# Performance work log

Hardware: AMD Instinct MI355X
Metric: run time of the kernel (lower is better)

## Reference

```python
import math
import jax, jax.numpy as jnp
import numpy as np

B, L, D = 2, 2048, 1024
NH = 16
HS = D // NH
BLOCK_SIZE = 2048


def setup_inputs() -> dict:
    key = jax.random.key(0)
    ks = jax.random.split(key, 4)
    x = jax.random.normal(ks[0], (B, L, D), dtype=jnp.float32)
    Wqkv = jax.random.normal(ks[1], (D, 3 * D), dtype=jnp.float32) * 0.02
    bqkv = jnp.zeros((3 * D,), dtype=jnp.float32)
    Wproj = jax.random.normal(ks[2], (D, D), dtype=jnp.float32) * 0.02
    bproj = jnp.zeros((D,), dtype=jnp.float32)
    Er = jax.random.normal(ks[3], (BLOCK_SIZE, HS), dtype=jnp.float32)
    return {"x": x, "Wqkv": Wqkv, "bqkv": bqkv, "Wproj": Wproj, "bproj": bproj, "Er": Er}


def _skew(QEr):
    # QEr: [B, nh, L, L]  (Music Transformer skew trick)
    b, nh, nr, nc = QEr.shape
    padded = jnp.pad(QEr, ((0, 0), (0, 0), (0, 0), (1, 0)))  # [B, nh, nr, nc+1]
    reshaped = padded.reshape(b, nh, nc + 1, nr)
    return reshaped[:, :, 1:, :]  # [B, nh, nr, nc]


def reference(x, Wqkv, bqkv, Wproj, bproj, Er):
    b, l, d = x.shape
    qkv = x @ Wqkv + bqkv  # [B, L, 3D]
    q, k, v = jnp.split(qkv, 3, axis=2)
    q = q.reshape(b, l, NH, HS).transpose(0, 2, 1, 3)  # [B, nh, L, hs]
    k = k.reshape(b, l, NH, HS).transpose(0, 2, 1, 3)
    v = v.reshape(b, l, NH, HS).transpose(0, 2, 1, 3)

    start = BLOCK_SIZE - l
    Er_t = Er[start:, :].T  # [hs, L]
    QEr = jnp.einsum('bhld,dm->bhlm', q, Er_t)  # [B, nh, L, L]
    Srel = _skew(QEr)

    QK_t = jnp.einsum('bhld,bhmd->bhlm', q, k)
    scale = 1.0 / math.sqrt(HS)
    att = (QK_t + Srel) * scale
    causal = jnp.tril(jnp.ones((l, l), dtype=bool))
    att = jnp.where(causal[None, None, :, :], att, jnp.float32(-jnp.inf))
    att = jax.nn.softmax(att, axis=-1)
    y = jnp.einsum('bhlm,bhmd->bhld', att, v)
    y = y.transpose(0, 2, 1, 3).reshape(b, l, d)
    return y @ Wproj + bproj
```

## Files before the change

kernel.cpp:

```cpp
#include <hip/hip_runtime.h>
#include <stdint.h>

#define BB 2
#define LL 2048
#define DD 1024
#define NHH 16
#define HSS 64

typedef __bf16 bf16x8 __attribute__((ext_vector_type(8)));
typedef float f32x4 __attribute__((ext_vector_type(4)));

__device__ __forceinline__ bf16x8 load8(const float* p) {
  float4 f0 = *(const float4*)p;
  float4 f1 = *(const float4*)(p + 4);
  bf16x8 v;
  v[0] = (__bf16)f0.x; v[1] = (__bf16)f0.y; v[2] = (__bf16)f0.z; v[3] = (__bf16)f0.w;
  v[4] = (__bf16)f1.x; v[5] = (__bf16)f1.y; v[6] = (__bf16)f1.z; v[7] = (__bf16)f1.w;
  return v;
}
__device__ __forceinline__ bf16x8 load8(const __bf16* p) {
  return *(const bf16x8*)p;
}

__device__ __forceinline__ void async_ld16(__bf16* lds_uniform_base,
                                           const __bf16* gptr_per_lane) {
  __builtin_amdgcn_global_load_lds(
      (const __attribute__((address_space(1))) void*)gptr_per_lane,
      (__attribute__((address_space(3))) void*)lds_uniform_base, 16, 0, 0);
}

__global__ void prep_k(const float* __restrict__ Wqkv, const float* __restrict__ x,
                       const float* __restrict__ Er, __bf16* __restrict__ WqkvT,
                       __bf16* __restrict__ xb, __bf16* __restrict__ Erb) {
  int tx = threadIdx.x, ty = threadIdx.y;
  int tid = ty * 32 + tx;
  if (blockIdx.z == 1) {
    if (blockIdx.x >= 2048) return;
    size_t off = ((size_t)blockIdx.x * 256 + tid) * 8;
    *(bf16x8*)&xb[off] = load8(&x[off]);
    return;
  }
  if (blockIdx.z == 2) {
    if (blockIdx.x >= 64) return;
    size_t off = ((size_t)blockIdx.x * 256 + tid) * 8;
    *(bf16x8*)&Erb[off] = load8(&Er[off]);
    return;
  }
  __shared__ __bf16 tile[32][33];
  int c0 = (blockIdx.x % 96) * 32, r0 = (blockIdx.x / 96) * 32;
#pragma unroll
  for (int i = ty; i < 32; i += 8)
    tile[i][tx] = (__bf16)Wqkv[(size_t)(r0 + i) * 3072 + c0 + tx];
  __syncthreads();
#pragma unroll
  for (int i = ty; i < 32; i += 8)
    WqkvT[(size_t)(c0 + i) * 1024 + r0 + tx] = tile[tx][i];
}

__global__ void tconv_k(const float* __restrict__ src, __bf16* __restrict__ dst,
                        int R, int C) {
  __shared__ __bf16 tile[32][33];
  int c0 = blockIdx.x * 32, r0 = blockIdx.y * 32;
  int tx = threadIdx.x, ty = threadIdx.y;
#pragma unroll
  for (int i = ty; i < 32; i += 8)
    tile[i][tx] = (__bf16)src[(size_t)(r0 + i) * C + c0 + tx];
  __syncthreads();
#pragma unroll
  for (int i = ty; i < 32; i += 8)
    dst[(size_t)(c0 + i) * R + r0 + tx] = tile[tx][i];
}

__global__ __launch_bounds__(256) void gemm_qkv_k(
    const __bf16* __restrict__ A, const __bf16* __restrict__ Bt,
    const float* __restrict__ bias, __bf16* __restrict__ Qo,
    __bf16* __restrict__ Ko, __bf16* __restrict__ Vto) {
  const int K = 1024;
  __shared__ __align__(16) __bf16 As[128 * 32];
  __shared__ __align__(16) __bf16 Bs[128 * 32];
  __shared__ __align__(16) __bf16 Vl[64 * 136];
  int t = threadIdx.x;
  int wave = t >> 6, lane = t & 63, qd = lane >> 4, lr = lane & 15;
  int m0 = blockIdx.y * 128, n0 = blockIdx.x * 128;
  int wm = (wave >> 1) * 64, wn = (wave & 1) * 64;
  f32x4 acc[4][4] = {};
  int srow = lane >> 2, sch = (lane & 3) * 8;
  const __bf16* Ab[2];
  const __bf16* Bb[2];
#pragma unroll
  for (int c = 0; c < 2; c++) {
    Ab[c] = A + (size_t)(m0 + (wave * 2 + c) * 16 + srow) * K + sch;
    Bb[c] = Bt + (size_t)(n0 + (wave * 2 + c) * 16 + srow) * K + sch;
  }
  for (int k0 = 0; k0 < K; k0 += 32) {
    __syncthreads();
#pragma unroll
    for (int c = 0; c < 2; c++) {
      async_ld16(&As[(wave * 2 + c) * 512], Ab[c] + k0);
      async_ld16(&Bs[(wave * 2 + c) * 512], Bb[c] + k0);
    }
    __syncthreads();
    bf16x8 af[4], bfr[4];
#pragma unroll
    for (int mt = 0; mt < 4; mt++)
      af[mt] = *(const bf16x8*)&As[(wm + mt * 16 + lr) * 32 + qd * 8];
#pragma unroll
    for (int nt = 0; nt < 4; nt++)
      bfr[nt] = *(const bf16x8*)&Bs[(wn + nt * 16 + lr) * 32 + qd * 8];
#pragma unroll
    for (int mt = 0; mt < 4; mt++)
#pragma unroll
      for (int nt = 0; nt < 4; nt++)
        acc[mt][nt] = __builtin_amdgcn_mfma_f32_16x16x32_bf16(af[mt], bfr[nt],
                                                              acc[mt][nt], 0, 0, 0);
  }
  float bvv[4];
#pragma unroll
  for (int nt = 0; nt < 4; nt++) bvv[nt] = bias[n0 + wn + nt * 16 + lr];

  if (n0 < 2 * DD) {
#pragma unroll
    for (int mt = 0; mt < 4; mt++)
#pragma unroll
      for (int nt = 0; nt < 4; nt++)
#pragma unroll
        for (int r = 0; r < 4; r++) {
          int row = m0 + wm + mt * 16 + qd * 4 + r;
          int col = n0 + wn + nt * 16 + lr;
          __bf16 bb = (__bf16)(acc[mt][nt][r] + bvv[nt]);
          int b = row >> 11, l = row & 2047;
          int h = (col >> 6) & 15, d = col & 63;
          if (col < DD) {
            Qo[(((size_t)(b * NHH + h)) * LL + l) * HSS + d] = bb;
          } else {
            Ko[(((size_t)(b * NHH + h)) * LL + l) * HSS + d] = bb;
          }
        }
  } else {
    int vb0 = n0 - 2 * DD;
    int bq = m0 >> 11, l0 = m0 & 2047;
    int vr = t >> 2, vc = (t & 3) * 8;
#pragma unroll
    for (int c = 0; c < 2; c++) {
      if ((wave & 1) == c) {
#pragma unroll
        for (int mt = 0; mt < 4; mt++)
#pragma unroll
          for (int nt = 0; nt < 4; nt++)
#pragma unroll
            for (int r = 0; r < 4; r++) {
              int vrow = nt * 16 + lr;
              int ml = wm + mt * 16 + qd * 4 + r;
              Vl[vrow * 136 + ml] = (__bf16)(acc[mt][nt][r] + bvv[nt]);
            }
      }
      __syncthreads();
      int h = (vb0 + c * 64) >> 6;
      __bf16* dst = Vto + (((size_t)(bq * NHH + h)) * HSS + vr) * LL + l0 + vc;
      const __bf16* src = &Vl[vr * 136 + vc];
#pragma unroll
      for (int u = 0; u < 4; u++)
        *(bf16x8*)(dst + u * 32) = *(const bf16x8*)(src + u * 32);
      __syncthreads();
    }
  }
}

__global__ __launch_bounds__(256) void gemm_proj_k(
    const __bf16* __restrict__ A, const __bf16* __restrict__ Bt,
    const float* __restrict__ bias, float* __restrict__ out) {
  const int K = 1024, N = 1024;
  __shared__ __align__(16) __bf16 As[128 * 32];
  __shared__ __align__(16) __bf16 Bs[64 * 32];
  int t = threadIdx.x;
  int wave = t >> 6, lane = t & 63, qd = lane >> 4, lr = lane & 15;
  int m0 = blockIdx.y * 128, n0 = blockIdx.x * 64;
  int wm = (wave >> 1) * 64, wn = (wave & 1) * 32;
  f32x4 acc[4][2] = {};
  int srow = lane >> 2, sch = (lane & 3) * 8;
  const __bf16* Ab[2];
  const __bf16* Bb;
#pragma unroll
  for (int c = 0; c < 2; c++)
    Ab[c] = A + (size_t)(m0 + (wave * 2 + c) * 16 + srow) * K + sch;
  Bb = Bt + (size_t)(n0 + wave * 16 + srow) * K + sch;

  for (int k0 = 0; k0 < K; k0 += 32) {
    __syncthreads();
#pragma unroll
    for (int c = 0; c < 2; c++)
      async_ld16(&As[(wave * 2 + c) * 512], Ab[c] + k0);
    async_ld16(&Bs[wave * 512], Bb + k0);
    __syncthreads();
    bf16x8 af[4], bfr[2];
#pragma unroll
    for (int mt = 0; mt < 4; mt++)
      af[mt] = *(const bf16x8*)&As[(wm + mt * 16 + lr) * 32 + qd * 8];
#pragma unroll
    for (int nt = 0; nt < 2; nt++)
      bfr[nt] = *(const bf16x8*)&Bs[(wn + nt * 16 + lr) * 32 + qd * 8];
#pragma unroll
    for (int mt = 0; mt < 4; mt++)
#pragma unroll
      for (int nt = 0; nt < 2; nt++)
        acc[mt][nt] = __builtin_amdgcn_mfma_f32_16x16x32_bf16(af[mt], bfr[nt],
                                                              acc[mt][nt], 0, 0, 0);
  }
  float bvv[2];
#pragma unroll
  for (int nt = 0; nt < 2; nt++) bvv[nt] = bias[n0 + wn + nt * 16 + lr];
#pragma unroll
  for (int mt = 0; mt < 4; mt++)
#pragma unroll
    for (int nt = 0; nt < 2; nt++)
#pragma unroll
      for (int r = 0; r < 4; r++) {
        int row = m0 + wm + mt * 16 + qd * 4 + r;
        int col = n0 + wn + nt * 16 + lr;
        out[(size_t)row * N + col] = acc[mt][nt][r] + bvv[nt];
      }
}

__global__ __launch_bounds__(256, 3) void flash_k(
    const __bf16* __restrict__ Qg, const __bf16* __restrict__ Kg,
    const __bf16* __restrict__ Vtg, const __bf16* __restrict__ Erb,
    __bf16* __restrict__ Po0, __bf16* __restrict__ Po1,
    float* __restrict__ Lp0, float* __restrict__ Lp1) {
  __shared__ __align__(16) __bf16 Kbuf[2][64 * 64];
  __shared__ __align__(16) __bf16 Vbuf[2][64 * 64];
  __shared__ __align__(16) __bf16 Pball[4][16 * 64];

  int bh = blockIdx.x;
  int tile = 31 - (int)blockIdx.y;
  int i0 = tile * 64;
  int niter = tile + 1;
  int mid = (niter + 1) >> 1;
  int it0 = (blockIdx.z == 0) ? 0 : mid;
  int it1 = (blockIdx.z == 0) ? mid : niter;
  const __bf16* Qh = Qg + (size_t)bh * LL * HSS;
  const __bf16* Kh = Kg + (size_t)bh * LL * HSS;
  const __bf16* Vth = Vtg + (size_t)bh * HSS * LL;
  int b = bh >> 4, h = bh & 15;
  int t = threadIdx.x, wave = t >> 6, lane = t & 63, qd = lane >> 4, lr = lane & 15;
  __bf16* Pb = &Pball[wave][0];
  int cbase = 48 - wave * 16;

  const float SC = 0.18033688011112042f;

  int lrow = lane >> 3;
  int lcol = ((lane & 7) ^ lrow) * 8;
  const __bf16* KsrcB[2];
  const __bf16* VsrcB[2];
#pragma unroll
  for (int c = 0; c < 2; c++) {
    int q = wave * 2 + c;
    KsrcB[c] = Kh + (size_t)(q * 8 + lrow) * HSS + lcol;
    VsrcB[c] = Vth + (size_t)(q * 8 + lrow) * LL + lcol;
  }

  int swA = (qd ^ (lr & 7)) * 8;
  int swB = ((qd + 4) ^ (lr & 7)) * 8;

  int hi8 = lr >> 3;
  int ib0 = 15 - qd * 4 + lr;
  int pb0 = qd * 256 + (lr & 7);
  int px0 = (qd & 1) * 4;
  int rowb = i0 + wave * 16 + qd * 4;

  bf16x8 aq[2];
  {
    const __bf16* qrow = Qh + (size_t)(i0 + wave * 16 + lr) * HSS + qd * 8;
    aq[0] = *(const bf16x8*)qrow;
    aq[1] = *(const bf16x8*)(qrow + 32);
  }
  f32x4 oacc[4] = {};
  float lsum[4] = {};

  int cur = 0;
  if (it0 < it1) {
    int j0 = it0 * 64;
#pragma unroll
    for (int c = 0; c < 2; c++) {
      async_ld16(&Kbuf[0][(wave * 2 + c) * 512], KsrcB[c] + (size_t)j0 * HSS);
      async_ld16(&Vbuf[0][(wave * 2 + c) * 512], VsrcB[c] + j0);
    }
  }
  __syncthreads();

  for (int it = it0; it < it1; ++it) {
    int j0 = it * 64;

    if (it + 1 < it1) {
      int jn = (it + 1) * 64;
#pragma unroll
      for (int c = 0; c < 2; c++) {
        async_ld16(&Kbuf[cur ^ 1][(wave * 2 + c) * 512], KsrcB[c] + (size_t)jn * HSS);
        async_ld16(&Vbuf[cur ^ 1][(wave * 2 + c) * 512], VsrcB[c] + jn);
      }
    }

    int ebase = LL - 64 - i0 + j0 + cbase + lr;
    int e[5];
#pragma unroll
    for (int ct = 0; ct < 5; ct++) {
      int v = ebase + ct * 16;
      e[ct] = (v < LL) ? v : (LL - 1);
    }
    bf16x8 ef[5];
#pragma unroll
    for (int ct = 0; ct < 5; ct++)
      ef[ct] = *(const bf16x8*)&Erb[(size_t)e[ct] * HSS + qd * 8];

    const __bf16* Kb = &Kbuf[cur][0];
    const __bf16* Vb = &Vbuf[cur][0];

    f32x4 sacc[4] = {};
    __builtin_amdgcn_s_setprio(1);
#pragma unroll
    for (int ct = 0; ct < 4; ct++) {
      bf16x8 bk0 = *(const bf16x8*)&Kb[(ct * 16 + lr) * 64 + swA];
      bf16x8 bk1 = *(const bf16x8*)&Kb[(ct * 16 + lr) * 64 + swB];
      sacc[ct] = __builtin_amdgcn_mfma_f32_16x16x32_bf16(aq[0], bk0, sacc[ct], 0, 0, 0);
      sacc[ct] = __builtin_amdgcn_mfma_f32_16x16x32_bf16(aq[1], bk1, sacc[ct], 0, 0, 0);
    }
    __builtin_amdgcn_s_setprio(0);

    f32x4 racc[5] = {};
    __builtin_amdgcn_s_setprio(1);
#pragma unroll
    for (int ct = 0; ct < 5; ct++)
      racc[ct] = __builtin_amdgcn_mfma_f32_16x16x32_bf16(aq[0], ef[ct], racc[ct], 0, 0, 0);
    __builtin_amdgcn_s_setprio(0);

    __builtin_amdgcn_sched_barrier(0);

#pragma unroll
    for (int ct = 0; ct < 5; ct++)
      ef[ct] = *(const bf16x8*)&Erb[(size_t)e[ct] * HSS + 32 + qd * 8];

    __builtin_amdgcn_s_setprio(1);
#pragma unroll
    for (int ct = 0; ct < 5; ct++)
      racc[ct] = __builtin_amdgcn_mfma_f32_16x16x32_bf16(aq[1], ef[ct], racc[ct], 0, 0, 0);
    __builtin_amdgcn_s_setprio(0);

    int dib = rowb - j0;
#pragma unroll
    for (int r = 0; r < 4; r++) {
      int bse = ib0 - r;
      int hi = bse >> 4;
      int idx = (qd * 16 + (bse & 15)) << 2;
      float sh[5];
#pragma unroll
      for (int ct = 0; ct < 5; ct++)
        sh[ct] = __int_as_float(
            __builtin_amdgcn_ds_bpermute(idx, __float_as_int(racc[ct][r])));
      int di = dib + r;
#pragma unroll
      for (int ct2 = 0; ct2 < 4; ct2++) {
        float rel = hi ? sh[ct2 + 1] : sh[ct2];
        float p = __builtin_exp2f((sacc[ct2][r] + rel) * SC);
        p = (ct2 * 16 + lr <= di) ? p : 0.f;
        __bf16 pb = (__bf16)p;
        lsum[r] += (float)pb;
        Pb[pb0 + r * 64 + (((2 * ct2 + hi8) ^ (px0 + r)) << 3)] = pb;
      }
    }

    bf16x8 ap0 = *(const bf16x8*)&Pb[lr * 64 + swA];
    bf16x8 ap1 = *(const bf16x8*)&Pb[lr * 64 + swB];
    __builtin_amdgcn_s_setprio(1);
#pragma unroll
    for (int dt = 0; dt < 4; dt++) {
      bf16x8 bv0 = *(const bf16x8*)&Vb[(dt * 16 + lr) * 64 + swA];
      bf16x8 bv1 = *(const bf16x8*)&Vb[(dt * 16 + lr) * 64 + swB];
      oacc[dt] = __builtin_amdgcn_mfma_f32_16x16x32_bf16(ap0, bv0, oacc[dt], 0, 0, 0);
      oacc[dt] = __builtin_amdgcn_mfma_f32_16x16x32_bf16(ap1, bv1, oacc[dt], 0, 0, 0);
    }
    __builtin_amdgcn_s_setprio(0);

    __syncthreads();
    cur ^= 1;
  }

#pragma unroll
  for (int r = 0; r < 4; r++) {
#pragma unroll
    for (int m = 1; m < 16; m <<= 1)
      lsum[r] += __shfl_xor(lsum[r], m, 64);
  }

  __bf16* Po = (blockIdx.z == 0) ? Po0 : Po1;
  float* Lp = (blockIdx.z == 0) ? Lp0 : Lp1;
#pragma unroll
  for (int r = 0; r < 4; r++) {
    int l = i0 + wave * 16 + qd * 4 + r;
    if (lr == 0) Lp[(size_t)bh * LL + l] = lsum[r];
#pragma unroll
    for (int dt = 0; dt < 4; dt++) {
      int d = dt * 16 + lr;
      Po[((size_t)(b * LL) + l) * DD + h * HSS + d] = (__bf16)oacc[dt][r];
    }
  }
}

__global__ void combine_k(const __bf16* __restrict__ Po0,
                          const __bf16* __restrict__ Po1,
                          const float* __restrict__ Lp0,
                          const float* __restrict__ Lp1,
                          __bf16* __restrict__ Y) {
  size_t f = ((size_t)blockIdx.x * 256 + threadIdx.x) * 8;
  int dfull = (int)(f & 1023);
  int h = dfull >> 6;
  int l = (int)((f >> 10) & 2047);
  int b = (int)(f >> 21);
  size_t lidx = ((size_t)(b * NHH + h)) * LL + l;
  float linv = 1.f / (Lp0[lidx] + Lp1[lidx]);
  bf16x8 a = *(const bf16x8*)&Po0[f];
  bf16x8 c = *(const bf16x8*)&Po1[f];
  bf16x8 o;
#pragma unroll
  for (int q = 0; q < 8; q++)
    o[q] = (__bf16)(((float)a[q] + (float)c[q]) * linv);
  *(bf16x8*)&Y[f] = o;
}

extern "C" void kernel_launch(void* const* d_in, const int* in_sizes, int n_in,
                              void* d_out, int out_size, void* d_ws, size_t ws_size,
                              hipStream_t stream) {
  const float* x = (const float*)d_in[0];
  const float* Wqkv = (const float*)d_in[1];
  const float* bqkv = (const float*)d_in[2];
  const float* Wproj = (const float*)d_in[3];
  const float* bproj = (const float*)d_in[4];
  const float* Er = (const float*)d_in[5];
  float* out = (float*)d_out;

  if (ws_size < 4u * 8388608u) return;

  uint8_t* w = (uint8_t*)d_ws;
  __bf16* Q = (__bf16*)w;  w += (size_t)BB * NHH * LL * HSS * 2;
  __bf16* Kt = (__bf16*)w; w += (size_t)BB * NHH * LL * HSS * 2;
  __bf16* Vt = (__bf16*)w; w += (size_t)BB * NHH * LL * HSS * 2;
  __bf16* Y = (__bf16*)w;  w += (size_t)BB * LL * DD * 2;

  __bf16* WqkvT = (__bf16*)d_out;
  __bf16* xb = (__bf16*)((uint8_t*)d_out + (size_t)3072 * 1024 * 2);
  __bf16* Erb = (__bf16*)((uint8_t*)d_out + (size_t)3072 * 1024 * 2 + (size_t)4096 * 1024 * 2);
  __bf16* Po1 = (__bf16*)d_out;
  float* Lp0 = (float*)((uint8_t*)d_out + (size_t)BB * LL * DD * 2);
  float* Lp1 = (float*)((uint8_t*)d_out + (size_t)BB * LL * DD * 2 + (size_t)BB * NHH * LL * 4);
  __bf16* Po0 = Y;
  __bf16* WprojT = Q;

  prep_k<<<dim3(3072, 1, 3), dim3(32, 8), 0, stream>>>(Wqkv, x, Er, WqkvT, xb, Erb);
  gemm_qkv_k<<<dim3(3072 / 128, 4096 / 128), 256, 0, stream>>>(
      xb, WqkvT, bqkv, Q, Kt, Vt);
  flash_k<<<dim3(BB * NHH, 32, 2), 256, 0, stream>>>(
      Q, Kt, Vt, Erb, Po0, Po1, Lp0, Lp1);
  combine_k<<<dim3(2048), 256, 0, stream>>>(Po0, Po1, Lp0, Lp1, Y);
  tconv_k<<<dim3(1024 / 32, 1024 / 32), dim3(32, 8), 0, stream>>>(Wproj, WprojT, 1024, 1024);
  gemm_proj_k<<<dim3(1024 / 64, 4096 / 128), 256, 0, stream>>>(Y, WprojT, bproj, out);
}
```

Before: 243.6 us.

## Fuse split-KV combine into flash kernel via atomic last-block counter

Removes the separate combine kernel. Each flash block now bumps a per-(head, tile) atomic counter, and the second finisher merges the two partial outputs and sums in place into Po0. The counters are zeroed inside prep_k in a spare region of the output buffer. The Er fragment loads are also reorganized so both halves are issued early, and the sched_barrier between the two relative-position MFMA groups is removed. This saves one kernel launch and a full pass over memory, at the cost of atomics, threadfences and more register pressure.

```diff
diff --git a/kernel.cpp b/kernel.cpp
--- a/kernel.cpp
+++ b/kernel.cpp
@@ -31,7 +31,8 @@
 
 __global__ void prep_k(const float* __restrict__ Wqkv, const float* __restrict__ x,
                        const float* __restrict__ Er, __bf16* __restrict__ WqkvT,
-                       __bf16* __restrict__ xb, __bf16* __restrict__ Erb) {
+                       __bf16* __restrict__ xb, __bf16* __restrict__ Erb,
+                       int* __restrict__ cnt) {
   int tx = threadIdx.x, ty = threadIdx.y;
   int tid = ty * 32 + tx;
   if (blockIdx.z == 1) {
@@ -41,7 +42,12 @@
     return;
   }
   if (blockIdx.z == 2) {
-    if (blockIdx.x >= 64) return;
+    if (blockIdx.x == 64) {
+      int4 z4; z4.x = 0; z4.y = 0; z4.z = 0; z4.w = 0;
+      ((int4*)cnt)[tid] = z4;
+      return;
+    }
+    if (blockIdx.x > 64) return;
     size_t off = ((size_t)blockIdx.x * 256 + tid) * 8;
     *(bf16x8*)&Erb[off] = load8(&Er[off]);
     return;
@@ -224,8 +230,9 @@
 __global__ __launch_bounds__(256, 3) void flash_k(
     const __bf16* __restrict__ Qg, const __bf16* __restrict__ Kg,
     const __bf16* __restrict__ Vtg, const __bf16* __restrict__ Erb,
-    __bf16* __restrict__ Po0, __bf16* __restrict__ Po1,
-    float* __restrict__ Lp0, float* __restrict__ Lp1) {
+    __bf16* Po0, __bf16* __restrict__ Po1,
+    float* __restrict__ Lp0, float* __restrict__ Lp1,
+    int* __restrict__ cnt) {
   __shared__ __align__(16) __bf16 Kbuf[2][64 * 64];
   __shared__ __align__(16) __bf16 Vbuf[2][64 * 64];
   __shared__ __align__(16) __bf16 Pball[4][16 * 64];
@@ -306,10 +313,10 @@
       int v = ebase + ct * 16;
       e[ct] = (v < LL) ? v : (LL - 1);
     }
-    bf16x8 ef[5];
+    bf16x8 ef0[5];
 #pragma unroll
     for (int ct = 0; ct < 5; ct++)
-      ef[ct] = *(const bf16x8*)&Erb[(size_t)e[ct] * HSS + qd * 8];
+      ef0[ct] = *(const bf16x8*)&Erb[(size_t)e[ct] * HSS + qd * 8];
 
     const __bf16* Kb = &Kbuf[cur][0];
     const __bf16* Vb = &Vbuf[cur][0];
@@ -325,23 +332,19 @@
     }
     __builtin_amdgcn_s_setprio(0);
 
+    bf16x8 ef1[5];
+#pragma unroll
+    for (int ct = 0; ct < 5; ct++)
+      ef1[ct] = *(const bf16x8*)&Erb[(size_t)e[ct] * HSS + 32 + qd * 8];
+
     f32x4 racc[5] = {};
     __builtin_amdgcn_s_setprio(1);
 #pragma unroll
     for (int ct = 0; ct < 5; ct++)
-      racc[ct] = __builtin_amdgcn_mfma_f32_16x16x32_bf16(aq[0], ef[ct], racc[ct], 0, 0, 0);
-    __builtin_amdgcn_s_setprio(0);
-
-    __builtin_amdgcn_sched_barrier(0);
-
+      racc[ct] = __builtin_amdgcn_mfma_f32_16x16x32_bf16(aq[0], ef0[ct], racc[ct], 0, 0, 0);
 #pragma unroll
     for (int ct = 0; ct < 5; ct++)
-      ef[ct] = *(const bf16x8*)&Erb[(size_t)e[ct] * HSS + 32 + qd * 8];
-
-    __builtin_amdgcn_s_setprio(1);
-#pragma unroll
-    for (int ct = 0; ct < 5; ct++)
-      racc[ct] = __builtin_amdgcn_mfma_f32_16x16x32_bf16(aq[1], ef[ct], racc[ct], 0, 0, 0);
+      racc[ct] = __builtin_amdgcn_mfma_f32_16x16x32_bf16(aq[1], ef1[ct], racc[ct], 0, 0, 0);
     __builtin_amdgcn_s_setprio(0);
 
     int dib = rowb - j0;
@@ -402,27 +405,29 @@
       Po[((size_t)(b * LL) + l) * DD + h * HSS + d] = (__bf16)oacc[dt][r];
     }
   }
-}
-
-__global__ void combine_k(const __bf16* __restrict__ Po0,
-                          const __bf16* __restrict__ Po1,
-                          const float* __restrict__ Lp0,
-                          const float* __restrict__ Lp1,
-                          __bf16* __restrict__ Y) {
-  size_t f = ((size_t)blockIdx.x * 256 + threadIdx.x) * 8;
-  int dfull = (int)(f & 1023);
-  int h = dfull >> 6;
-  int l = (int)((f >> 10) & 2047);
-  int b = (int)(f >> 21);
-  size_t lidx = ((size_t)(b * NHH + h)) * LL + l;
-  float linv = 1.f / (Lp0[lidx] + Lp1[lidx]);
-  bf16x8 a = *(const bf16x8*)&Po0[f];
-  bf16x8 c = *(const bf16x8*)&Po1[f];
-  bf16x8 o;
-#pragma unroll
-  for (int q = 0; q < 8; q++)
-    o[q] = (__bf16)(((float)a[q] + (float)c[q]) * linv);
-  *(bf16x8*)&Y[f] = o;
+
+  __threadfence();
+  __shared__ int lastf;
+  if (t == 0) lastf = atomicAdd(&cnt[bh * 32 + tile], 1);
+  __syncthreads();
+  if (lastf == 1) {
+    __threadfence();
+    int r8 = t >> 3, c8 = (t & 7) * 8;
+#pragma unroll
+    for (int rr = 0; rr < 64; rr += 32) {
+      int l = i0 + r8 + rr;
+      size_t lidx = (size_t)bh * LL + l;
+      float linv = 1.f / (Lp0[lidx] + Lp1[lidx]);
+      size_t off = ((size_t)(b * LL) + l) * DD + h * HSS + c8;
+      bf16x8 a = *(const bf16x8*)&Po0[off];
+      bf16x8 c = *(const bf16x8*)&Po1[off];
+      bf16x8 o;
+#pragma unroll
+      for (int q = 0; q < 8; q++)
+        o[q] = (__bf16)(((float)a[q] + (float)c[q]) * linv);
+      *(bf16x8*)&Po0[off] = o;
+    }
+  }
 }
 
 extern "C" void kernel_launch(void* const* d_in, const int* in_sizes, int n_in,
@@ -450,15 +455,15 @@
   __bf16* Po1 = (__bf16*)d_out;
   float* Lp0 = (float*)((uint8_t*)d_out + (size_t)BB * LL * DD * 2);
   float* Lp1 = (float*)((uint8_t*)d_out + (size_t)BB * LL * DD * 2 + (size_t)BB * NHH * LL * 4);
+  int* cnt = (int*)((uint8_t*)d_out + (size_t)3072 * 1024 * 2 + (size_t)4096 * 1024 * 2 + (size_t)2048 * 64 * 2);
   __bf16* Po0 = Y;
   __bf16* WprojT = Q;
 
-  prep_k<<<dim3(3072, 1, 3), dim3(32, 8), 0, stream>>>(Wqkv, x, Er, WqkvT, xb, Erb);
+  prep_k<<<dim3(3072, 1, 3), dim3(32, 8), 0, stream>>>(Wqkv, x, Er, WqkvT, xb, Erb, cnt);
   gemm_qkv_k<<<dim3(3072 / 128, 4096 / 128), 256, 0, stream>>>(
       xb, WqkvT, bqkv, Q, Kt, Vt);
   flash_k<<<dim3(BB * NHH, 32, 2), 256, 0, stream>>>(
-      Q, Kt, Vt, Erb, Po0, Po1, Lp0, Lp1);
-  combine_k<<<dim3(2048), 256, 0, stream>>>(Po0, Po1, Lp0, Lp1, Y);
+      Q, Kt, Vt, Erb, Po0, Po1, Lp0, Lp1, cnt);
   tconv_k<<<dim3(1024 / 32, 1024 / 32), dim3(32, 8), 0, stream>>>(Wproj, WprojT, 1024, 1024);
   gemm_proj_k<<<dim3(1024 / 64, 4096 / 128), 256, 0, stream>>>(Y, WprojT, bproj, out);
 }
```

After: 585.7 us. +140.5%, slower.
